# Performance work log

Measured on AMD Instinct MI355X. Metric: run time of the kernel, lower is better.

Reference implementation:

```python
import jax, jax.numpy as jnp
import numpy as np

B, N, M, D = 32, 1024, 1024, 128  # pairs, nodes in X-graph, nodes in Y-graph, feature dim


def setup_inputs() -> dict:
    key = jax.random.key(0)
    k0, k1, k2, k3 = jax.random.split(key, 4)
    return {
        "Xs": jax.random.normal(k0, (B, N, D), dtype=jnp.float32),
        "Ys": jax.random.normal(k1, (B, M, D), dtype=jnp.float32),
        "weights": jax.random.normal(k2, (B, N, D), dtype=jnp.float32),
        "A_w": jax.random.normal(k3, (D, D), dtype=jnp.float32) / np.sqrt(D).astype(np.float32),
        "A_b": jnp.zeros((D,), dtype=jnp.float32),
    }


def reference(Xs, Ys, weights, A_w, A_b):
    # coefficients = tanh(Linear(W))  -> [B, N, D]
    coeff = jnp.tanh(jnp.einsum("bnd,ed->bne", weights, A_w) + A_b)
    # affinity: softplus((X * coeff) @ Y^T) - 0.5  -> [B, N, M]
    s = jax.nn.softplus(jnp.einsum("bnd,bmd->bnm", Xs * coeff, Ys)) - 0.5
    # dual-direction attention
    a_x = jax.nn.softmax(s, axis=2)   # row softmax (dim=1 on [N,M])
    a_y = jax.nn.softmax(s, axis=1)   # col softmax (dim=0 on [N,M])
    attention_x = jnp.einsum("bnm,bmd->bnd", a_x, Ys)   # a_x @ Y
    attention_y = jnp.einsum("bnm,bnd->bmd", a_y, Xs)   # a_y^T @ X
    return attention_x, attention_y, s
```

## Files before the change

### kernel.cpp

```cpp
#include <hip/hip_runtime.h>
#include <hip/hip_bf16.h>

#define BB 32
#define NN 1024
#define MM 1024
#define DD 128

typedef __bf16 bf16;
typedef bf16 bf16x8 __attribute__((ext_vector_type(8)));
typedef bf16 bf16x4 __attribute__((ext_vector_type(4)));
typedef float f32x4 __attribute__((ext_vector_type(4)));

#define LOG2E 1.4426950408889634f
#define LN2   0.6931471805599453f
#define ESHIFT 30.5f
#define ESHIFT_C 5.6757e-14f

__device__ __forceinline__ bf16x8 ld8(const bf16* p) {
    return *reinterpret_cast<const bf16x8*>(p);
}

__device__ __forceinline__ bf16x8 cvt8(const float* p) {
    float4 a = reinterpret_cast<const float4*>(p)[0];
    float4 c = reinterpret_cast<const float4*>(p)[1];
    bf16x8 r;
    r[0]=(bf16)a.x; r[1]=(bf16)a.y; r[2]=(bf16)a.z; r[3]=(bf16)a.w;
    r[4]=(bf16)c.x; r[5]=(bf16)c.y; r[6]=(bf16)c.z; r[7]=(bf16)c.w;
    return r;
}

__global__ __launch_bounds__(256) void k_prep(
    const float* __restrict__ Xs, const float* __restrict__ Ys,
    bf16* __restrict__ Ysb, bf16* __restrict__ YsT, bf16* __restrict__ XsT) {
    __shared__ float tile[64][65];
    int L = blockIdx.x;
    int xcd = L & 7, sidx = L >> 3;
    int b = xcd + 8 * (sidx & 3);
    int t = sidx >> 2;
    int isY = (t < 32);
    int tt = t & 31;
    int mtile = tt >> 1, dtile = tt & 1;
    int r0 = mtile * 64, d0 = dtile * 64;
    int tid = threadIdx.x;
    const float* src = (isY ? Ys : Xs) + (size_t)b * 1024 * DD;

    int rr = tid >> 4;
    int c4 = (tid & 15) * 4;
#pragma unroll
    for (int p = 0; p < 4; ++p) {
        int row = p * 16 + rr;
        float4 v = *reinterpret_cast<const float4*>(src + (size_t)(r0 + row) * DD + d0 + c4);
        tile[row][c4] = v.x; tile[row][c4 + 1] = v.y;
        tile[row][c4 + 2] = v.z; tile[row][c4 + 3] = v.w;
        if (isY) {
            bf16x4 o; o[0] = (bf16)v.x; o[1] = (bf16)v.y; o[2] = (bf16)v.z; o[3] = (bf16)v.w;
            *reinterpret_cast<bf16x4*>(Ysb + (size_t)b * MM * DD + (size_t)(r0 + row) * DD + d0 + c4) = o;
        }
    }
    __syncthreads();
    bf16* dT = (isY ? YsT : XsT) + (size_t)b * DD * 1024;
#pragma unroll
    for (int q = 0; q < 2; ++q) {
        int d = q * 32 + (tid >> 3);
        int m0 = (tid & 7) * 8;
        bf16x8 o;
#pragma unroll
        for (int j = 0; j < 8; ++j) o[j] = (bf16)tile[m0 + j][d];
        *reinterpret_cast<bf16x8*>(dT + (size_t)(d0 + d) * 1024 + r0 + m0) = o;
    }
}

__global__ __launch_bounds__(256) void k_coeff(
    const float* __restrict__ Xs, const float* __restrict__ W,
    const float* __restrict__ Aw, const float* __restrict__ Ab,
    bf16* __restrict__ Xc) {
    __shared__ bf16 cf[64][136];
    int L = blockIdx.x;
    int xcd = L & 7, sidx = L >> 3;
    int b = xcd + 8 * (sidx & 3);
    int ntile = sidx >> 2;
    int tid = threadIdx.x;
    int w = tid >> 6, lane = tid & 63, quad = lane >> 4, l16 = lane & 15;
    int nbase = ntile * 64 + w * 16;

    f32x4 accZ[8];
#pragma unroll
    for (int ef = 0; ef < 8; ++ef) accZ[ef] = {0.f, 0.f, 0.f, 0.f};

    const float* Wb = W + ((size_t)b * NN + nbase + l16) * DD;
#pragma unroll
    for (int ks = 0; ks < 4; ++ks) {
        bf16x8 aW = cvt8(Wb + ks * 32 + quad * 8);
#pragma unroll
        for (int ef = 0; ef < 8; ++ef) {
            bf16x8 bA = cvt8(Aw + (size_t)(ef * 16 + l16) * DD + ks * 32 + quad * 8);
            accZ[ef] = __builtin_amdgcn_mfma_f32_16x16x32_bf16(aW, bA, accZ[ef], 0, 0, 0);
        }
    }
#pragma unroll
    for (int ef = 0; ef < 8; ++ef) {
        float ab = Ab[ef * 16 + l16];
#pragma unroll
        for (int r = 0; r < 4; ++r) {
            float z = accZ[ef][r] + ab;
            z = fminf(fmaxf(z, -12.f), 12.f);
            float t = __builtin_amdgcn_exp2f(z * (2.f * LOG2E));
            float c = (t - 1.f) / (t + 1.f);
            cf[w * 16 + quad * 4 + r][ef * 16 + l16] = (bf16)c;
        }
    }
    __syncthreads();
    const float* Xs_b = Xs + ((size_t)b * NN + ntile * 64) * DD;
    bf16* Xc_b = Xc + ((size_t)b * NN + ntile * 64) * DD;
    int row = tid >> 4, colg = (tid & 15) * 8;
#pragma unroll
    for (int p = 0; p < 4; ++p) {
        int rrow = p * 16 + row;
        float4 xa = *reinterpret_cast<const float4*>(Xs_b + (size_t)rrow * DD + colg);
        float4 xb = *reinterpret_cast<const float4*>(Xs_b + (size_t)rrow * DD + colg + 4);
        bf16x8 cv = *reinterpret_cast<const bf16x8*>(&cf[rrow][colg]);
        bf16x8 o;
        o[0] = (bf16)(xa.x * (float)cv[0]); o[1] = (bf16)(xa.y * (float)cv[1]);
        o[2] = (bf16)(xa.z * (float)cv[2]); o[3] = (bf16)(xa.w * (float)cv[3]);
        o[4] = (bf16)(xb.x * (float)cv[4]); o[5] = (bf16)(xb.y * (float)cv[5]);
        o[6] = (bf16)(xb.z * (float)cv[6]); o[7] = (bf16)(xb.w * (float)cv[7]);
        *reinterpret_cast<bf16x8*>(Xc_b + (size_t)rrow * DD + colg) = o;
    }
}

__global__ __launch_bounds__(256, 2) void k_main(
    const bf16* __restrict__ Xc, const bf16* __restrict__ Ysb,
    const bf16* __restrict__ YsT, const bf16* __restrict__ XsT,
    float* __restrict__ out_x, float* __restrict__ out_y,
    float* __restrict__ out_s) {
    __shared__ __align__(16) bf16 stage[2][16384];
    __shared__ __align__(16) bf16 Et[4][16][72];

    int L = blockIdx.x + 32 * blockIdx.y;
    int xcd = L & 7, sidx = L >> 3;
    int b = xcd + 8 * (sidx & 3);
    int t = sidx >> 2;
    int role = t >> 4, tile = t & 15;
    int tid = threadIdx.x;
    int w = tid >> 6, lane = tid & 63, quad = lane >> 4, l16 = lane & 15;
    int rbase = tile * 64 + w * 16;

    const bf16* Arow  = (role == 0 ? Xc : Ysb) + ((size_t)b * 1024 + rbase + l16) * DD;
    const bf16* Bmat  = (role == 0 ? Ysb : Xc) + (size_t)b * 1024 * DD;
    const bf16* BTmat = (role == 0 ? YsT : XsT) + (size_t)b * DD * 1024;
    float* s_b = out_s + (size_t)b * NN * MM;
    float* outp = (role == 0 ? out_x : out_y);

    bf16x8 aX[4];
#pragma unroll
    for (int ks = 0; ks < 4; ++ks) aX[ks] = ld8(Arow + ks * 32 + quad * 8);

    int isA = (w < 2);
    uint32_t wroff[8], soff[8];
#pragma unroll
    for (int i = 0; i < 8; ++i) {
        uint32_t o = (uint32_t)(w * 8 + i) * 1024 + (uint32_t)lane * 16;
        if (isA) {
            wroff[i] = o ^ (((o >> 8) & 7) << 4);
            soff[i]  = o;
        } else {
            uint32_t j = o - 16384;
            wroff[i] = 16384 + (j ^ (((j >> 7) & 7) << 4));
            soff[i]  = (j >> 7) * 2048 + (j & 127);
        }
    }
    const char* srcbase = (const char*)(isA ? Bmat : BTmat);
    uint32_t tstride = isA ? 16384u : 128u;

    bf16x8 stg[8];
#pragma unroll
    for (int i = 0; i < 8; ++i)
        stg[i] = *reinterpret_cast<const bf16x8*>(srcbase + soff[i]);
#pragma unroll
    for (int i = 0; i < 8; ++i)
        *reinterpret_cast<bf16x8*>((char*)&stage[0][0] + wroff[i]) = stg[i];
    __syncthreads();

    f32x4 accU[8];
#pragma unroll
    for (int df = 0; df < 8; ++df) accU[df] = {0.f, 0.f, 0.f, 0.f};
    float rowsum[4] = {0.f, 0.f, 0.f, 0.f};
    uint32_t xq = (uint32_t)(l16 & 7) << 4;
    int cur = 0;

#pragma unroll 1
    for (int tt = 0; tt < 16; ++tt) {
        if (tt < 15) {
#pragma unroll
            for (int i = 0; i < 8; ++i)
                stg[i] = *reinterpret_cast<const bf16x8*>(srcbase + (size_t)(tt + 1) * tstride + soff[i]);
        }
        __builtin_amdgcn_sched_barrier(0);

        const char* sb = (const char*)&stage[cur][0];
        f32x4 accS[4];
#pragma unroll
        for (int mf = 0; mf < 4; ++mf) accS[mf] = {0.f, 0.f, 0.f, 0.f};
#pragma unroll
        for (int ks = 0; ks < 4; ++ks) {
            bf16x8 bY[4];
#pragma unroll
            for (int mf = 0; mf < 4; ++mf)
                bY[mf] = *reinterpret_cast<const bf16x8*>(
                    sb + (uint32_t)(mf * 16 + l16) * 256 + (((uint32_t)(ks * 64 + quad * 16)) ^ xq));
#pragma unroll
            for (int mf = 0; mf < 4; ++mf)
                accS[mf] = __builtin_amdgcn_mfma_f32_16x16x32_bf16(aX[ks], bY[mf], accS[mf], 0, 0, 0);
        }
#pragma unroll
        for (int mf = 0; mf < 4; ++mf) {
#pragma unroll
            for (int r = 0; r < 4; ++r) {
                float x = accS[mf][r];
                float E = __builtin_amdgcn_exp2f((x - ESHIFT) * LOG2E) + ESHIFT_C;
                bf16 Eb = (bf16)E;
                rowsum[r] += (float)Eb;
                Et[w][quad * 4 + r][mf * 16 + l16] = Eb;
            }
            if (role == 0) {
#pragma unroll
                for (int r = 0; r < 4; ++r) {
                    float x = accS[mf][r];
                    float ax = fabsf(x);
                    float sp = fmaxf(x, 0.f) +
                               LN2 * __builtin_amdgcn_logf(1.f + __builtin_amdgcn_exp2f(-ax * LOG2E));
                    s_b[(size_t)(rbase + quad * 4 + r) * MM + tt * 64 + mf * 16 + l16] = sp - 0.5f;
                }
            }
        }
#pragma unroll
        for (int half = 0; half < 2; ++half) {
            bf16x8 aE = *reinterpret_cast<const bf16x8*>(&Et[w][l16][half * 32 + quad * 8]);
            bf16x8 bT[8];
#pragma unroll
            for (int df = 0; df < 8; ++df)
                bT[df] = *reinterpret_cast<const bf16x8*>(
                    sb + 16384 + (uint32_t)(df * 16 + l16) * 128 + (((uint32_t)(half * 64 + quad * 16)) ^ xq));
#pragma unroll
            for (int df = 0; df < 8; ++df)
                accU[df] = __builtin_amdgcn_mfma_f32_16x16x32_bf16(aE, bT[df], accU[df], 0, 0, 0);
        }
        __builtin_amdgcn_sched_barrier(0);
        if (tt < 15) {
#pragma unroll
            for (int i = 0; i < 8; ++i)
                *reinterpret_cast<bf16x8*>((char*)&stage[cur ^ 1][0] + wroff[i]) = stg[i];
        }
        __builtin_amdgcn_sched_barrier(0);
        asm volatile("s_waitcnt lgkmcnt(0)" ::: "memory");
        __builtin_amdgcn_s_barrier();
        __builtin_amdgcn_sched_barrier(0);
        cur ^= 1;
    }

    float inv[4];
#pragma unroll
    for (int r = 0; r < 4; ++r) {
        float rs = rowsum[r];
        rs += __shfl_xor(rs, 1); rs += __shfl_xor(rs, 2);
        rs += __shfl_xor(rs, 4); rs += __shfl_xor(rs, 8);
        inv[r] = 1.f / rs;
    }
#pragma unroll
    for (int df = 0; df < 8; ++df)
#pragma unroll
        for (int r = 0; r < 4; ++r)
            outp[((size_t)b * 1024 + rbase + quad * 4 + r) * DD + df * 16 + l16] = accU[df][r] * inv[r];
}

extern "C" void kernel_launch(void* const* d_in, const int* in_sizes, int n_in,
                              void* d_out, int out_size, void* d_ws, size_t ws_size,
                              hipStream_t stream) {
    const float* Xs = (const float*)d_in[0];
    const float* Ys = (const float*)d_in[1];
    const float* W  = (const float*)d_in[2];
    const float* Aw = (const float*)d_in[3];
    const float* Ab = (const float*)d_in[4];

    char* ws = (char*)d_ws;
    bf16*  Xc     = (bf16*)(ws);
    bf16*  Ysb    = (bf16*)(ws + 8388608);
    bf16*  YsT    = (bf16*)(ws + 16777216);
    bf16*  XsT    = (bf16*)(ws + 25165824);

    float* out_x = (float*)d_out;
    float* out_y = out_x + (size_t)BB * NN * DD;
    float* out_s = out_y + (size_t)BB * MM * DD;

    k_prep<<<dim3(2048), 256, 0, stream>>>(Xs, Ys, Ysb, YsT, XsT);
    k_coeff<<<dim3(512), 256, 0, stream>>>(Xs, W, Aw, Ab, Xc);
    k_main<<<dim3(32, BB), 256, 0, stream>>>(Xc, Ysb, YsT, XsT, out_x, out_y, out_s);
}
```

Baseline: 279.9 us.

## Stage B tiles via global_load_lds and derive softplus from the shifted exponential

Replaces register-staged global loads plus LDS stores with direct global-to-LDS loads (`__builtin_amdgcn_global_load_lds`). To keep the bank-conflict-avoiding layout, the XOR swizzle moves from the LDS write address to the global source offset. The loop barrier now waits on vmcnt instead of lgkmcnt. Softplus is also rewritten as ln(E) + ESHIFT - 0.5, reusing the already-computed shifted exponential, so each element needs one log instead of an extra exp, log and abs/max. The trade-off is that the vmcnt wait now also covers the outstanding s stores, and the softplus value depends on the fp32 precision of E.

```diff
diff --git a/kernel.cpp b/kernel.cpp
--- a/kernel.cpp
+++ b/kernel.cpp
@@ -15,6 +15,9 @@
 #define LN2   0.6931471805599453f
 #define ESHIFT 30.5f
 #define ESHIFT_C 5.6757e-14f
+
+typedef __attribute__((address_space(1))) const void gvoid_t;
+typedef __attribute__((address_space(3))) void lvoid_t;
 
 __device__ __forceinline__ bf16x8 ld8(const bf16* p) {
     return *reinterpret_cast<const bf16x8*>(p);
@@ -156,30 +159,38 @@
     for (int ks = 0; ks < 4; ++ks) aX[ks] = ld8(Arow + ks * 32 + quad * 8);
 
     int isA = (w < 2);
-    uint32_t wroff[8], soff[8];
+    uint32_t gsoff[8];
 #pragma unroll
     for (int i = 0; i < 8; ++i) {
         uint32_t o = (uint32_t)(w * 8 + i) * 1024 + (uint32_t)lane * 16;
         if (isA) {
-            wroff[i] = o ^ (((o >> 8) & 7) << 4);
-            soff[i]  = o;
+            gsoff[i] = o ^ (((o >> 8) & 7) << 4);
         } else {
             uint32_t j = o - 16384;
-            wroff[i] = 16384 + (j ^ (((j >> 7) & 7) << 4));
-            soff[i]  = (j >> 7) * 2048 + (j & 127);
+            gsoff[i] = (j >> 7) * 2048 + ((j & 127) ^ (((j >> 7) & 7) << 4));
         }
     }
     const char* srcbase = (const char*)(isA ? Bmat : BTmat);
     uint32_t tstride = isA ? 16384u : 128u;
 
-    bf16x8 stg[8];
-#pragma unroll
-    for (int i = 0; i < 8; ++i)
-        stg[i] = *reinterpret_cast<const bf16x8*>(srcbase + soff[i]);
-#pragma unroll
-    for (int i = 0; i < 8; ++i)
-        *reinterpret_cast<bf16x8*>((char*)&stage[0][0] + wroff[i]) = stg[i];
-    __syncthreads();
+#define STAGE_ISSUE(buf, tt_)                                                        \
+    do {                                                                             \
+        const char* gsb_ = srcbase + (size_t)(tt_) * tstride;                        \
+        _Pragma("unroll")                                                            \
+        for (int i_ = 0; i_ < 8; ++i_) {                                             \
+            __builtin_amdgcn_global_load_lds(                                        \
+                (gvoid_t*)(gsb_ + gsoff[i_]),                                        \
+                (lvoid_t*)((__attribute__((address_space(3))) char*)                 \
+                               ((char*)&stage[buf][0]) + (uint32_t)(w * 8 + i_) * 1024), \
+                16, 0, 0);                                                           \
+        }                                                                            \
+    } while (0)
+
+    STAGE_ISSUE(0, 0);
+    asm volatile("s_waitcnt vmcnt(0)" ::: "memory");
+    __builtin_amdgcn_sched_barrier(0);
+    __builtin_amdgcn_s_barrier();
+    __builtin_amdgcn_sched_barrier(0);
 
     f32x4 accU[8];
 #pragma unroll
@@ -190,11 +201,7 @@
 
 #pragma unroll 1
     for (int tt = 0; tt < 16; ++tt) {
-        if (tt < 15) {
-#pragma unroll
-            for (int i = 0; i < 8; ++i)
-                stg[i] = *reinterpret_cast<const bf16x8*>(srcbase + (size_t)(tt + 1) * tstride + soff[i]);
-        }
+        if (tt < 15) STAGE_ISSUE(cur ^ 1, tt + 1);
         __builtin_amdgcn_sched_barrier(0);
 
         const char* sb = (const char*)&stage[cur][0];
@@ -221,15 +228,9 @@
                 bf16 Eb = (bf16)E;
                 rowsum[r] += (float)Eb;
                 Et[w][quad * 4 + r][mf * 16 + l16] = Eb;
-            }
-            if (role == 0) {
-#pragma unroll
-                for (int r = 0; r < 4; ++r) {
-                    float x = accS[mf][r];
-                    float ax = fabsf(x);
-                    float sp = fmaxf(x, 0.f) +
-                               LN2 * __builtin_amdgcn_logf(1.f + __builtin_amdgcn_exp2f(-ax * LOG2E));
-                    s_b[(size_t)(rbase + quad * 4 + r) * MM + tt * 64 + mf * 16 + l16] = sp - 0.5f;
+                if (role == 0) {
+                    float sp = fmaf(LN2, __builtin_amdgcn_logf(E), ESHIFT - 0.5f);
+                    s_b[(size_t)(rbase + quad * 4 + r) * MM + tt * 64 + mf * 16 + l16] = sp;
                 }
             }
         }
@@ -246,17 +247,13 @@
                 accU[df] = __builtin_amdgcn_mfma_f32_16x16x32_bf16(aE, bT[df], accU[df], 0, 0, 0);
         }
         __builtin_amdgcn_sched_barrier(0);
-        if (tt < 15) {
-#pragma unroll
-            for (int i = 0; i < 8; ++i)
-                *reinterpret_cast<bf16x8*>((char*)&stage[cur ^ 1][0] + wroff[i]) = stg[i];
-        }
-        __builtin_amdgcn_sched_barrier(0);
-        asm volatile("s_waitcnt lgkmcnt(0)" ::: "memory");
+        asm volatile("s_waitcnt vmcnt(0)" ::: "memory");
+        __builtin_amdgcn_sched_barrier(0);
         __builtin_amdgcn_s_barrier();
         __builtin_amdgcn_sched_barrier(0);
         cur ^= 1;
     }
+#undef STAGE_ISSUE
 
     float inv[4];
 #pragma unroll
```

Measured after the change: 281.1 us. Within noise of the previous version (+0.4%).
